# Optimization experiments

Measured on AMD Instinct MI355X. Metric: run time of the kernel, lower is better.

Reference implementation:

```python
import jax, jax.numpy as jnp
import numpy as np

ARCH = (1024, 2048, 2048, 512)
STEPS = 20
LR = 0.1
BATCH = 4096


def setup_inputs() -> dict:
    key = jax.random.key(0)
    ks = jax.random.split(key, 1 + len(ARCH) - 1)
    x = jax.random.normal(ks[0], (BATCH, ARCH[0]), dtype=jnp.float32)
    inp = {"x": x}
    # forward layers: weight (out, in) as in torch nn.Linear, orthogonal-ish init gain sqrt(2)
    for i in range(len(ARCH) - 1):
        fan_in = ARCH[i]
        W = jax.random.normal(ks[1 + i], (ARCH[i + 1], fan_in), dtype=jnp.float32) * jnp.sqrt(2.0 / fan_in)
        inp[f"W{i}"] = W
        inp[f"b{i}"] = jnp.zeros((ARCH[i + 1],), dtype=jnp.float32)
    return inp


def _errors(r, Ws):
    # errors[-1] = r[-1]; errors[i] = r[i] - tanh(F.linear(r[i+1], W_i.T)) = r[i] - tanh(r[i+1] @ W_i)
    errs = [None] * len(ARCH)
    errs[-1] = r[-1]
    for i in range(len(Ws) - 1, -1, -1):
        errs[i] = r[i] - jnp.tanh(r[i + 1] @ Ws[i])  # (B, arch[i])
    return errs


def _pc_forward(x, Ws, bs):
    # initialize states with a no-grad feedforward pass (torch.no_grad -> stop_gradient)
    r = [x]
    t = x
    for W, b in zip(Ws, bs):
        t = jnp.tanh(t @ W.T + b)
        r.append(jax.lax.stop_gradient(t))

    def step(carry, _):
        r = list(carry)
        errs = _errors(r, Ws)
        new_r = [r[0]]  # r[0] = x, fixed
        for i in range(1, len(ARCH)):
            feedback = errs[i - 1] @ Ws[i - 1].T  # F.linear(errors[i-1], W)
            new_r.append(r[i] + LR * (-errs[i] + feedback))
        return tuple(new_r), None

    r, _ = jax.lax.scan(step, tuple(r), None, length=STEPS)
    r = list(r)
    final_errs = _errors(r, Ws)
    total_error = 0.5 * sum(jnp.sum(e * e) for e in final_errs)
    return r[-1], total_error


def reference(x, W0, b0, W1, b1, W2, b2):
    Ws = [W0, W1, W2]
    bs = [b0, b1, b2]
    return _pc_forward(x, Ws, bs)
```

## Files before the change

### kernel.cpp

```cpp
#include <hip/hip_runtime.h>

typedef unsigned short u16;
typedef __bf16 bf16_t;
typedef bf16_t bf16x8 __attribute__((ext_vector_type(8)));
typedef u16 u16x8 __attribute__((ext_vector_type(8)));
typedef float f32x4 __attribute__((ext_vector_type(4)));

__device__ __forceinline__ u16 f2bf(float f) {
    unsigned u = __builtin_bit_cast(unsigned, f);
    u += 0x7fffu + ((u >> 16) & 1u);
    return (u16)(u >> 16);
}
__device__ __forceinline__ float bf2f(u16 h) {
    unsigned u = ((unsigned)h) << 16;
    return __builtin_bit_cast(float, u);
}
__device__ __forceinline__ float fast_tanh(float x) {
    x = fminf(fmaxf(x, -20.f), 20.f);
    float e = __expf(2.f * x);
    return (e - 1.f) * __builtin_amdgcn_rcpf(e + 1.f);
}

__device__ __forceinline__ void gload_lds16(const void* g, void* l) {
    __builtin_amdgcn_global_load_lds((__attribute__((address_space(1))) void*)(g),
                                     (__attribute__((address_space(3))) void*)(l),
                                     16, 0, 0);
}



__global__ void cvt_bf16(const float* __restrict__ src, u16* __restrict__ dst, int n4) {
    int i = blockIdx.x * blockDim.x + threadIdx.x;
    if (i < n4) {
        float4 v = ((const float4*)src)[i];
        ushort4 o;
        o.x = f2bf(v.x); o.y = f2bf(v.y); o.z = f2bf(v.z); o.w = f2bf(v.w);
        ((ushort4*)dst)[i] = o;
    }
}

__global__ void transpose_cvt(const float* __restrict__ W, u16* __restrict__ WT, int R, int C) {
    __shared__ float tile[32][33];
    int c0 = blockIdx.x * 32, r0 = blockIdx.y * 32;
    int tx = threadIdx.x & 31, ty = threadIdx.x >> 5;
#pragma unroll
    for (int i = 0; i < 32; i += 8)
        tile[ty + i][tx] = W[(size_t)(r0 + ty + i) * C + (c0 + tx)];
    __syncthreads();
#pragma unroll
    for (int i = 0; i < 32; i += 8)
        WT[(size_t)(c0 + ty + i) * R + (r0 + tx)] = f2bf(tile[tx][ty + i]);
}

__global__ void blockify(const u16* __restrict__ src, u16* __restrict__ dst, int K) {
    const int nk = K >> 5;
    const int rb = blockIdx.x / nk, cb = blockIdx.x % nk;
    const int t = threadIdx.x;
    const int kloc = (t & 7) * 4;
    u16* d = dst + (size_t)blockIdx.x * 4096 + ((kloc >> 3) << 10) + (kloc & 7);
    const u16* s = src + (size_t)(rb * 128) * K + cb * 32 + kloc;
#pragma unroll
    for (int p = 0; p < 4; ++p) {
        int row = (t >> 3) + p * 32;
        *(ushort4*)(d + row * 8) = *(const ushort4*)(s + (size_t)row * K);
    }
}


struct Seg {
    const u16* A; const u16* B;
    const u16* rsrcb;
    const float* rsrcf;
    const float* bias;
    const u16* esub;
    float* outf;
    u16* outbf;
    int K, N, blkStart, mode, accum;
};
struct Phase {
    Seg seg[3];
    int bEnd0, bEnd1;
};

__global__ __launch_bounds__(256, 4) void pc_phase(Phase ph, float* __restrict__ errAcc) {
    __shared__ u16 As[4096];
    __shared__ u16 Bs[4096];
    __shared__ float red[4];

    const int bid = blockIdx.x;
    const int segi = (bid >= ph.bEnd0 ? 1 : 0) + (bid >= ph.bEnd1 ? 1 : 0);

    const int local = bid - ph.seg[segi].blkStart;
    const int bx = local >> 5;
    const int by = local & 31;
    const int K = ph.seg[segi].K;

    const int tid  = threadIdx.x;
    const int wave = tid >> 6, lane = tid & 63;
    const int q    = lane >> 4, ln = lane & 15;
    const int wrow = (wave >> 1) * 64, wcol = (wave & 1) * 64;

    const int nk = K >> 5;
    const u16* tA = ph.seg[segi].A + (size_t)by * nk * 4096 + wave * 1024 + lane * 8;
    const u16* tB = ph.seg[segi].B + (size_t)bx * nk * 4096 + wave * 1024 + lane * 8;
    u16* lA0 = &As[wave * 1024];
    u16* lA1 = &As[wave * 1024 + 512];
    u16* lB0 = &Bs[wave * 1024];
    u16* lB1 = &Bs[wave * 1024 + 512];

    f32x4 acc[4][4];
#pragma unroll
    for (int i = 0; i < 4; ++i)
#pragma unroll
        for (int j = 0; j < 4; ++j)
            acc[i][j] = (f32x4){0.f, 0.f, 0.f, 0.f};

    const u16* asrd = &As[q * 1024 + (wrow + ln) * 8];
    const u16* bsrd = &Bs[q * 1024 + (wcol + ln) * 8];

    for (int k = 0; k < nk; ++k) {
        const size_t kb = (size_t)k * 4096;
        gload_lds16(tA + kb, lA0);
        gload_lds16(tA + kb + 512, lA1);
        gload_lds16(tB + kb, lB0);
        gload_lds16(tB + kb + 512, lB1);
        __syncthreads();

        bf16x8 a[4], b[4];
#pragma unroll
        for (int mt = 0; mt < 4; ++mt)
            a[mt] = __builtin_bit_cast(bf16x8, *(const u16x8*)&asrd[mt * 128]);
#pragma unroll
        for (int nt = 0; nt < 4; ++nt)
            b[nt] = __builtin_bit_cast(bf16x8, *(const u16x8*)&bsrd[nt * 128]);
#pragma unroll
        for (int mt = 0; mt < 4; ++mt)
#pragma unroll
            for (int nt = 0; nt < 4; ++nt)
                acc[mt][nt] = __builtin_amdgcn_mfma_f32_16x16x32_bf16(
                    a[mt], b[nt], acc[mt][nt], 0, 0, 0);
        __syncthreads();
    }

    const int N = ph.seg[segi].N;
    const int mode = ph.seg[segi].mode;
    const int accum = ph.seg[segi].accum;
    const u16* rsrcb = ph.seg[segi].rsrcb;
    const float* rsrcf = ph.seg[segi].rsrcf;
    const float* bias = ph.seg[segi].bias;
    const u16* esub = ph.seg[segi].esub;
    float* outf = ph.seg[segi].outf;
    u16* outbf = ph.seg[segi].outbf;

    const int rowA0 = by * 128;
    const int rowB0 = bx * 128;
    const size_t regionOff = ((size_t)by * (N >> 5) + bx * 4) * 4096;
    const u16* rsrcR = rsrcb ? rsrcb + regionOff : nullptr;
    const u16* esubR = esub ? esub + regionOff : nullptr;
    u16* outR = outbf + regionOff;

    const int o0 = tid * 16;
    const int ch = o0 >> 8;
    const size_t gq = (size_t)(ch >> 2) * 4096 + (size_t)(ch & 3) * 1024 + (o0 & 255);

    float lsum = 0.f;
    const int myHalf = wave >> 1;

#pragma unroll
    for (int qq = 0; qq < 4; ++qq) {
        const size_t g = gq + qq * 256;
        if (mode == 1 || mode == 2) {
            *(u16x8*)(As + o0)     = *(const u16x8*)(rsrcR + g);
            *(u16x8*)(As + o0 + 8) = *(const u16x8*)(rsrcR + g + 8);
        }
        if (mode == 2) {
            *(u16x8*)(Bs + o0)     = *(const u16x8*)(esubR + g);
            *(u16x8*)(Bs + o0 + 8) = *(const u16x8*)(esubR + g + 8);
        }
        __syncthreads();

        if ((qq >> 1) == myHalf) {
            const int mtlo = (qq & 1) * 2;
#pragma unroll
            for (int mi = 0; mi < 2; ++mi) {
                const int mt = mtlo + mi;
#pragma unroll
                for (int r = 0; r < 4; ++r) {
                    const int rl = mi * 16 + q * 4 + r;
                    const int m = rowA0 + wrow + mt * 16 + q * 4 + r;
#pragma unroll
                    for (int nt = 0; nt < 4; ++nt) {
                        const int nrel = wcol + nt * 16 + ln;
                        const int o = (nrel >> 3) * 256 + rl * 8 + (nrel & 7);
                        const float c = acc[mt][nt][r];
                        float v;
                        if (mode == 0) {
                            v = fast_tanh(c + bias[rowB0 + nrel]);
                            if (outf) outf[(size_t)m * N + rowB0 + nrel] = v;
                        } else if (mode == 1) {
                            v = bf2f(As[o]) - fast_tanh(c);
                            if (accum) lsum += v * v;
                        } else if (mode == 2) {
                            v = bf2f(As[o]) + 0.1f * (c - bf2f(Bs[o]));
                        } else {
                            const size_t idx = (size_t)m * N + rowB0 + nrel;
                            v = 0.9f * rsrcf[idx] + 0.1f * c;
                            outf[idx] = v;
                            if (accum) lsum += v * v;
                        }
                        As[o] = f2bf(v);
                    }
                }
            }
        }
        __syncthreads();
        *(u16x8*)(outR + g)     = *(const u16x8*)(As + o0);
        *(u16x8*)(outR + g + 8) = *(const u16x8*)(As + o0 + 8);
        __syncthreads();
    }

    if (accum) {
        lsum *= 0.5f;
#pragma unroll
        for (int o = 32; o > 0; o >>= 1) lsum += __shfl_down(lsum, o);
        if (lane == 0) red[wave] = lsum;
        __syncthreads();
        if (tid == 0) atomicAdd(errAcc, red[0] + red[1] + red[2] + red[3]);
    }
}


extern "C" void kernel_launch(void* const* d_in, const int* in_sizes, int n_in,
                              void* d_out, int out_size, void* d_ws, size_t ws_size,
                              hipStream_t stream) {
    const float* x  = (const float*)d_in[0];
    const float* W0 = (const float*)d_in[1];
    const float* b0 = (const float*)d_in[2];
    const float* W1 = (const float*)d_in[3];
    const float* b1 = (const float*)d_in[4];
    const float* W2 = (const float*)d_in[5];
    const float* b2 = (const float*)d_in[6];

    const int Bz = 4096;

    char* ws = (char*)d_ws;
    size_t off = 0;
    auto alloc = [&](size_t bytes) -> char* {
        char* p = ws + off;
        off += (bytes + 255) & ~(size_t)255;
        return p;
    };

    u16*   r1b = (u16*)  alloc((size_t)Bz * 2048 * 2);
    u16*   r2b = (u16*)  alloc((size_t)Bz * 2048 * 2);
    u16*   r3b = (u16*)  alloc((size_t)Bz * 512 * 2);
    u16*   e0b = (u16*)  alloc((size_t)Bz * 1024 * 2);
    u16*   e1b = (u16*)  alloc((size_t)Bz * 2048 * 2);
    u16*   e2b = (u16*)  alloc((size_t)Bz * 2048 * 2);
    u16*   xb  = (u16*)  alloc((size_t)Bz * 1024 * 2);
    u16*   W0b = (u16*)  alloc((size_t)2048 * 1024 * 2);
    u16*   W0t = (u16*)  alloc((size_t)1024 * 2048 * 2);
    u16*   W1b = (u16*)  alloc((size_t)2048 * 2048 * 2);
    u16*   W1t = (u16*)  alloc((size_t)2048 * 2048 * 2);
    u16*   W2b = (u16*)  alloc((size_t)512 * 2048 * 2);
    u16*   W2t = (u16*)  alloc((size_t)2048 * 512 * 2);
    u16*   tmp = (u16*)  alloc((size_t)2048 * 2048 * 2);

    float* r3f    = (float*)d_out;
    float* errAcc = ((float*)d_out) + (size_t)Bz * 512;

    auto blkify = [&](const u16* s, u16* d, int M, int K) {
        blockify<<<(M / 128) * (K / 32), 256, 0, stream>>>(s, d, K);
    };

    cvt_bf16<<<(Bz * 1024 / 4) / 256, 256, 0, stream>>>(x, tmp, Bz * 1024 / 4);
    blkify(tmp, xb, Bz, 1024);
    cvt_bf16<<<(2048 * 1024 / 4) / 256, 256, 0, stream>>>(W0, tmp, 2048 * 1024 / 4);
    blkify(tmp, W0b, 2048, 1024);
    cvt_bf16<<<(2048 * 2048 / 4) / 256, 256, 0, stream>>>(W1, tmp, 2048 * 2048 / 4);
    blkify(tmp, W1b, 2048, 2048);
    cvt_bf16<<<(512 * 2048 / 4) / 256, 256, 0, stream>>>(W2, tmp, 512 * 2048 / 4);
    blkify(tmp, W2b, 512, 2048);
    transpose_cvt<<<dim3(1024 / 32, 2048 / 32), 256, 0, stream>>>(W0, tmp, 2048, 1024);
    blkify(tmp, W0t, 1024, 2048);
    transpose_cvt<<<dim3(2048 / 32, 2048 / 32), 256, 0, stream>>>(W1, tmp, 2048, 2048);
    blkify(tmp, W1t, 2048, 2048);
    transpose_cvt<<<dim3(2048 / 32, 512 / 32),  256, 0, stream>>>(W2, tmp, 512, 2048);
    blkify(tmp, W2t, 2048, 512);

    hipMemsetAsync(errAcc, 0, 4, stream);

    auto mkseg = [&](const u16* A, const u16* B, int K, int N,
                     const u16* rsrcb, const float* rsrcf, const float* bias,
                     const u16* esub, float* outf, u16* outbf,
                     int mode, int accum) {
        Seg s;
        s.A = A; s.B = B; s.rsrcb = rsrcb; s.rsrcf = rsrcf; s.bias = bias;
        s.esub = esub; s.outf = outf; s.outbf = outbf;
        s.K = K; s.N = N; s.blkStart = 0; s.mode = mode; s.accum = accum;
        return s;
    };
    auto nblk = [&](int N) { return (N / 128) * (Bz / 128); };

    auto launch1 = [&](Seg s0) {
        Phase ph;
        int b0 = nblk(s0.N);
        ph.seg[0] = s0; ph.seg[1] = s0; ph.seg[2] = s0;
        ph.bEnd0 = b0; ph.bEnd1 = b0;
        pc_phase<<<b0, 256, 0, stream>>>(ph, errAcc);
    };
    auto launch3 = [&](Seg s0, Seg s1, Seg s2) {
        Phase ph;
        int b0 = nblk(s0.N), b1 = nblk(s1.N), b2 = nblk(s2.N);
        s1.blkStart = b0; s2.blkStart = b0 + b1;
        ph.seg[0] = s0; ph.seg[1] = s1; ph.seg[2] = s2;
        ph.bEnd0 = b0; ph.bEnd1 = b0 + b1;
        pc_phase<<<b0 + b1 + b2, 256, 0, stream>>>(ph, errAcc);
    };

    launch1(mkseg(xb,  W0b, 1024, 2048, nullptr, nullptr, b0, nullptr, nullptr, r1b, 0, 0));
    launch1(mkseg(r1b, W1b, 2048, 2048, nullptr, nullptr, b1, nullptr, nullptr, r2b, 0, 0));
    launch1(mkseg(r2b, W2b, 2048, 512,  nullptr, nullptr, b2, nullptr, r3f,     r3b, 0, 0));

    for (int s = 0; s < 20; ++s) {
        int last = (s == 19) ? 1 : 0;
        launch3(mkseg(r2b, W1t, 2048, 2048, r1b, nullptr, nullptr, nullptr, nullptr, e1b, 1, 0),
                mkseg(r1b, W0t, 2048, 1024, xb,  nullptr, nullptr, nullptr, nullptr, e0b, 1, 0),
                mkseg(r3b, W2t, 512,  2048, r2b, nullptr, nullptr, nullptr, nullptr, e2b, 1, 0));
        launch3(mkseg(e1b, W1b, 2048, 2048, r2b, nullptr, nullptr, e2b, nullptr, r2b, 2, 0),
                mkseg(e2b, W2b, 2048, 512,  nullptr, r3f, nullptr, nullptr, r3f,  r3b, 3, last),
                mkseg(e0b, W0b, 1024, 2048, r1b, nullptr, nullptr, e1b, nullptr, r1b, 2, 0));
    }

    launch3(mkseg(r2b, W1t, 2048, 2048, r1b, nullptr, nullptr, nullptr, nullptr, e1b, 1, 1),
            mkseg(r1b, W0t, 2048, 1024, xb,  nullptr, nullptr, nullptr, nullptr, e0b, 1, 1),
            mkseg(r3b, W2t, 512,  2048, r2b, nullptr, nullptr, nullptr, nullptr, e2b, 1, 1));
}
```

Baseline: 4.097 ms.

## Double-buffer LDS tiles with async global_load_lds prefetch two stages ahead

Doubles the A/B shared-memory tiles and issues direct-to-LDS global loads for tiles k+1 and k+2 ahead of compute. Explicit vmcnt waits and raw barriers replace __syncthreads, so the next tile's loads can overlap the current tile's MFMAs. LDS use doubles to 32KB per block, which may reduce occupancy below the 4 blocks per CU in the launch bounds. The epilogue reuses the first buffer as its staging image.

```diff
diff --git a/kernel.cpp b/kernel.cpp
--- a/kernel.cpp
+++ b/kernel.cpp
@@ -26,6 +26,9 @@
                                      (__attribute__((address_space(3))) void*)(l),
                                      16, 0, 0);
 }
+
+#define WAITCNT_VM4 0x3F74
+#define WAITCNT_VM0 0x3F70
 
 
 
@@ -83,8 +86,8 @@
 };
 
 __global__ __launch_bounds__(256, 4) void pc_phase(Phase ph, float* __restrict__ errAcc) {
-    __shared__ u16 As[4096];
-    __shared__ u16 Bs[4096];
+    __shared__ u16 As[2][4096];
+    __shared__ u16 Bs[2][4096];
     __shared__ float red[4];
 
     const int bid = blockIdx.x;
@@ -103,10 +106,6 @@
     const int nk = K >> 5;
     const u16* tA = ph.seg[segi].A + (size_t)by * nk * 4096 + wave * 1024 + lane * 8;
     const u16* tB = ph.seg[segi].B + (size_t)bx * nk * 4096 + wave * 1024 + lane * 8;
-    u16* lA0 = &As[wave * 1024];
-    u16* lA1 = &As[wave * 1024 + 512];
-    u16* lB0 = &Bs[wave * 1024];
-    u16* lB1 = &Bs[wave * 1024 + 512];
 
     f32x4 acc[4][4];
 #pragma unroll
@@ -115,31 +114,47 @@
         for (int j = 0; j < 4; ++j)
             acc[i][j] = (f32x4){0.f, 0.f, 0.f, 0.f};
 
-    const u16* asrd = &As[q * 1024 + (wrow + ln) * 8];
-    const u16* bsrd = &Bs[q * 1024 + (wcol + ln) * 8];
+    auto issueTile = [&](int k, int buf) {
+        const size_t kb = (size_t)k * 4096;
+        gload_lds16(tA + kb,       &As[buf][wave * 1024]);
+        gload_lds16(tA + kb + 512, &As[buf][wave * 1024 + 512]);
+        gload_lds16(tB + kb,       &Bs[buf][wave * 1024]);
+        gload_lds16(tB + kb + 512, &Bs[buf][wave * 1024 + 512]);
+    };
+
+    issueTile(0, 0);
+    if (nk > 1) issueTile(1, 1);
+
+    const int ardo = q * 1024 + (wrow + ln) * 8;
+    const int brdo = q * 1024 + (wcol + ln) * 8;
 
     for (int k = 0; k < nk; ++k) {
-        const size_t kb = (size_t)k * 4096;
-        gload_lds16(tA + kb, lA0);
-        gload_lds16(tA + kb + 512, lA1);
-        gload_lds16(tB + kb, lB0);
-        gload_lds16(tB + kb + 512, lB1);
-        __syncthreads();
-
+        asm volatile("" ::: "memory");
+        if (k + 1 < nk) __builtin_amdgcn_s_waitcnt(WAITCNT_VM4);
+        else            __builtin_amdgcn_s_waitcnt(WAITCNT_VM0);
+        __builtin_amdgcn_s_barrier();
+        asm volatile("" ::: "memory");
+
+        const u16* as = &As[k & 1][ardo];
+        const u16* bs = &Bs[k & 1][brdo];
         bf16x8 a[4], b[4];
 #pragma unroll
         for (int mt = 0; mt < 4; ++mt)
-            a[mt] = __builtin_bit_cast(bf16x8, *(const u16x8*)&asrd[mt * 128]);
+            a[mt] = __builtin_bit_cast(bf16x8, *(const u16x8*)&as[mt * 128]);
 #pragma unroll
         for (int nt = 0; nt < 4; ++nt)
-            b[nt] = __builtin_bit_cast(bf16x8, *(const u16x8*)&bsrd[nt * 128]);
+            b[nt] = __builtin_bit_cast(bf16x8, *(const u16x8*)&bs[nt * 128]);
 #pragma unroll
         for (int mt = 0; mt < 4; ++mt)
 #pragma unroll
             for (int nt = 0; nt < 4; ++nt)
                 acc[mt][nt] = __builtin_amdgcn_mfma_f32_16x16x32_bf16(
                     a[mt], b[nt], acc[mt][nt], 0, 0, 0);
-        __syncthreads();
+
+        asm volatile("" ::: "memory");
+        __builtin_amdgcn_s_barrier();
+        asm volatile("" ::: "memory");
+        if (k + 2 < nk) issueTile(k + 2, k & 1);
     }
 
     const int N = ph.seg[segi].N;
@@ -159,6 +174,9 @@
     const u16* esubR = esub ? esub + regionOff : nullptr;
     u16* outR = outbf + regionOff;
 
+    u16* imgA = &As[0][0];
+    u16* imgB = &Bs[0][0];
+
     const int o0 = tid * 16;
     const int ch = o0 >> 8;
     const size_t gq = (size_t)(ch >> 2) * 4096 + (size_t)(ch & 3) * 1024 + (o0 & 255);
@@ -170,12 +188,12 @@
     for (int qq = 0; qq < 4; ++qq) {
         const size_t g = gq + qq * 256;
         if (mode == 1 || mode == 2) {
-            *(u16x8*)(As + o0)     = *(const u16x8*)(rsrcR + g);
-            *(u16x8*)(As + o0 + 8) = *(const u16x8*)(rsrcR + g + 8);
+            *(u16x8*)(imgA + o0)     = *(const u16x8*)(rsrcR + g);
+            *(u16x8*)(imgA + o0 + 8) = *(const u16x8*)(rsrcR + g + 8);
         }
         if (mode == 2) {
-            *(u16x8*)(Bs + o0)     = *(const u16x8*)(esubR + g);
-            *(u16x8*)(Bs + o0 + 8) = *(const u16x8*)(esubR + g + 8);
+            *(u16x8*)(imgB + o0)     = *(const u16x8*)(esubR + g);
+            *(u16x8*)(imgB + o0 + 8) = *(const u16x8*)(esubR + g + 8);
         }
         __syncthreads();
 
@@ -198,24 +216,24 @@
                             v = fast_tanh(c + bias[rowB0 + nrel]);
                             if (outf) outf[(size_t)m * N + rowB0 + nrel] = v;
                         } else if (mode == 1) {
-                            v = bf2f(As[o]) - fast_tanh(c);
+                            v = bf2f(imgA[o]) - fast_tanh(c);
                             if (accum) lsum += v * v;
                         } else if (mode == 2) {
-                            v = bf2f(As[o]) + 0.1f * (c - bf2f(Bs[o]));
+                            v = bf2f(imgA[o]) + 0.1f * (c - bf2f(imgB[o]));
                         } else {
                             const size_t idx = (size_t)m * N + rowB0 + nrel;
                             v = 0.9f * rsrcf[idx] + 0.1f * c;
                             outf[idx] = v;
                             if (accum) lsum += v * v;
                         }
-                        As[o] = f2bf(v);
+                        imgA[o] = f2bf(v);
                     }
                 }
             }
         }
         __syncthreads();
-        *(u16x8*)(outR + g)     = *(const u16x8*)(As + o0);
-        *(u16x8*)(outR + g + 8) = *(const u16x8*)(As + o0 + 8);
+        *(u16x8*)(outR + g)     = *(const u16x8*)(imgA + o0);
+        *(u16x8*)(outR + g + 8) = *(const u16x8*)(imgA + o0 + 8);
         __syncthreads();
     }
 
```

Measured after the change: 3.951 ms. 3.5% less time.
